# Optimization experiments

Hardware: AMD Instinct MI355X
Metric: run time of the kernel (lower is better)

Reference implementation:

```python
import jax, jax.numpy as jnp
import numpy as np

# --- constants mirroring ContextualAttention_Enhance defaults ---
C_IN = 64      # in_channels
C_I  = 16      # inter_channels
PS   = 7       # patch size (ps)
K    = 100     # top-k neighbors (k_s)
WS   = 21      # search window (ws)
S0   = 4       # query stride (stride0); stride1 = 1
SCALE = 10.0   # softmax_scale
B, H, W = 2, 96, 96
NH, NW = H // S0, W // S0
Q, HW, NC = NH * NW, H * W, WS * WS
P2, W2 = PS // 2, WS // 2


def _conv1x1(x, w, b):
    # x: [B,C,H,W], w: [Co,Ci], b: [Co]
    return jnp.einsum('bchw,oc->bohw', x, w) + b[None, :, None, None]


def _all_patches(x):
    # x: [C,H,W] -> centered ps x ps patches (clamped bounds) for every pixel: [HW, C*PS*PS]
    off = jnp.arange(PS) - P2
    ii = jnp.clip(jnp.arange(H)[:, None] + off, 0, H - 1)   # [H,PS]
    jj = jnp.clip(jnp.arange(W)[:, None] + off, 0, W - 1)   # [W,PS]
    p = x[:, ii[:, None, :, None], jj[None, :, None, :]]     # [C,H,W,PS,PS]
    return p.transpose(1, 2, 0, 3, 4).reshape(HW, -1)


def _query_pos():
    qi = jnp.repeat(jnp.arange(NH) * S0, NW)
    qj = jnp.tile(jnp.arange(NW) * S0, NH)
    return qi, qj


def _cand_idx():
    # flat pixel index of the WS x WS candidate centers around each query (clamped)
    qi, qj = _query_pos()
    d = jnp.arange(WS) - W2
    ci = jnp.clip(qi[:, None, None] + d[None, :, None], 0, H - 1)
    cj = jnp.clip(qj[:, None, None] + d[None, None, :], 0, W - 1)
    return (ci * W + cj).reshape(Q, NC)


def _attend(theta, phi, g):
    # theta/phi/g: [C_I,H,W]. Windowed top-k patch search + weighted patch-sum + fold.
    qi, qj = _query_pos()
    Qp = _all_patches(theta)[qi * W + qj]          # [Q, D] query patches
    Kp = _all_patches(phi)                          # [HW, D] key patches
    cand = _cand_idx()                              # [Q, NC]
    dfull = Qp @ Kp.T                               # [Q, HW] patch inner products
    dc = jnp.take_along_axis(dfull, cand, axis=1)   # [Q, NC] windowed scores
    topv, topi = jax.lax.top_k(dc, K)               # [Q, K]
    top = jnp.take_along_axis(cand, topi, axis=1)   # [Q, K] flat pixel inds
    wgt = jax.nn.softmax(SCALE * topv, axis=-1)     # [Q, K]
    Vp = _all_patches(g)                            # [HW, D] value patches
    z = jnp.einsum('qk,qkd->qd', wgt, Vp[top])      # weighted patch sum [Q, D]
    # fold: scatter-add patches back at query centers, normalize by overlap counts
    off = jnp.arange(PS) - P2
    pi = jnp.clip(qi[:, None, None] + off[:, None], 0, H - 1)
    pj = jnp.clip(qj[:, None, None] + off[None, :], 0, W - 1)
    pidx = (pi * W + pj).reshape(Q, PS * PS)
    zp = z.reshape(Q, C_I, PS * PS).transpose(1, 0, 2)        # [C_I,Q,PP]
    img = jnp.zeros((C_I, HW), z.dtype).at[:, pidx].add(zp)
    cnt = jnp.zeros((HW,), z.dtype).at[pidx.reshape(-1)].add(1.0)
    return (img / jnp.maximum(cnt, 1.0)[None]).reshape(C_I, H, W)


def setup_inputs() -> dict:
    key = jax.random.key(0)
    ks = jax.random.split(key, 12)
    s = 0.05
    return {
        'vid':     jax.random.normal(ks[0], (B, C_IN, H, W), jnp.float32),
        'w_theta': jax.random.normal(ks[1], (C_I, C_IN), jnp.float32) * s,
        'b_theta': jax.random.normal(ks[2], (C_I,), jnp.float32) * s,
        'w_phi':   jax.random.normal(ks[3], (C_I, C_IN), jnp.float32) * s,
        'b_phi':   jax.random.normal(ks[4], (C_I,), jnp.float32) * s,
        'w_g':     jax.random.normal(ks[5], (C_I, C_IN), jnp.float32) * s,
        'b_g':     jax.random.normal(ks[6], (C_I,), jnp.float32) * s,
        'w_w':     jax.random.normal(ks[7], (C_IN, C_I), jnp.float32) * s,
        'b_w':     jax.random.normal(ks[8], (C_IN,), jnp.float32) * s,
        'w_c33':   jax.random.normal(ks[9], (C_IN, 2 * C_IN), jnp.float32) * s,
        'b_c33':   jax.random.normal(ks[10], (C_IN,), jnp.float32) * s,
    }


def reference(vid, w_theta, b_theta, w_phi, b_phi, w_g, b_g, w_w, b_w, w_c33, b_c33):
    theta = _conv1x1(vid, w_theta, b_theta)   # [B,C_I,H,W]
    phi   = _conv1x1(vid, w_phi, b_phi)
    gval  = _conv1x1(vid, w_g, b_g)
    z = jax.vmap(_attend)(theta, phi, gval)   # [B,C_I,H,W]
    y = _conv1x1(z, w_w, b_w)                 # back to C_IN channels
    return _conv1x1(jnp.concatenate([y, vid], axis=1), w_c33, b_c33)
```

## Files before the change

kernel.cpp:

```cpp
#include <hip/hip_runtime.h>
#include <stdint.h>

typedef unsigned int u32;
typedef unsigned short u16;
typedef unsigned char u8;
typedef unsigned long long u64;
typedef _Float16 h2 __attribute__((ext_vector_type(2)));
typedef _Float16 h4 __attribute__((ext_vector_type(4)));
typedef _Float16 h8 __attribute__((ext_vector_type(8)));
typedef float f4 __attribute__((ext_vector_type(4)));

#define DEV __device__ __forceinline__

constexpr int HWp = 9216;

constexpr size_t O_I16 = 0;
constexpr size_t N_I16 = 2ull * 9216 * 48;
constexpr size_t O_Z   = O_I16 + N_I16 * 2;
constexpr size_t N_Z   = 2ull * 576 * 784;
constexpr size_t WS_NEED = O_Z + N_Z * 4;

DEV float bf2f(u16 x) { return __uint_as_float(((u32)x) << 16); }
DEV int clampi(int v, int lo, int hi) { return v < lo ? lo : (v > hi ? hi : v); }
DEV float cvt(const void* p, int i, bool f32) {
  return f32 ? ((const float*)p)[i] : bf2f(((const u16*)p)[i]);
}
DEV float dot2(h2 a, h2 b, float c) {
#if __has_builtin(__builtin_amdgcn_fdot2)
  return __builtin_amdgcn_fdot2(a, b, c, false);
#else
  return c + (float)a[0]*(float)b[0] + (float)a[1]*(float)b[1];
#endif
}
DEV float dot8(h8 a, h8 b, float c) {
  c = dot2(__builtin_shufflevector(a,a,0,1), __builtin_shufflevector(b,b,0,1), c);
  c = dot2(__builtin_shufflevector(a,a,2,3), __builtin_shufflevector(b,b,2,3), c);
  c = dot2(__builtin_shufflevector(a,a,4,5), __builtin_shufflevector(b,b,4,5), c);
  c = dot2(__builtin_shufflevector(a,a,6,7), __builtin_shufflevector(b,b,6,7), c);
  return c;
}
DEV bool hit256(const void* p, int tid) {
  u16 v = ((const u16*)p)[tid];
  return (((u32)v >> 7) & 0xFFu) >= 0xC8u;
}

__global__ __launch_bounds__(256, 2) void k1_conv(const void* vid, const void* wth, const void* bth,
    const void* wph, const void* bph, const void* wg, const void* bg, u8* ws)
{
  __shared__ float vidL[64 * 65];
  __shared__ float wL[48 * 65];
  __shared__ float bL[48];
  __shared__ __align__(16) _Float16 outL[64 * 48];
  __shared__ int redL[8];
  int tid = threadIdx.x;
  int g0 = blockIdx.x * 64;
  int b = g0 / HWp, px0 = g0 % HWp;

  {
    u64 b1 = __ballot(hit256(vid, tid));
    u64 b2 = __ballot(hit256(wth, tid));
    if ((tid & 63) == 0) { redL[tid >> 6] = __popcll(b1); redL[4 + (tid >> 6)] = __popcll(b2); }
  }
  __syncthreads();
  const bool vf = (redL[0] + redL[1] + redL[2] + redL[3]) >= 4;
  const bool wf = (redL[4] + redL[5] + redL[6] + redL[7]) >= 4;

  if (wf) {
    for (int e = tid; e < 768; e += 256) {
      int a = e >> 8, j = e & 255;
      int o = j >> 4, c4 = (j & 15) << 2;
      const float* src = (a == 0) ? (const float*)wth : (a == 1) ? (const float*)wph : (const float*)wg;
      f4 x = *(const f4*)(src + o*64 + c4);
#pragma unroll
      for (int jj = 0; jj < 4; ++jj) wL[(a*16 + o)*65 + c4 + jj] = x[jj];
    }
  } else {
    for (int e = tid; e < 384; e += 256) {
      int a = e >> 7, j = e & 127;
      int o = j >> 5, c2 = (j & 31) << 1;
      const u16* src = (a == 0) ? (const u16*)wth : (a == 1) ? (const u16*)wph : (const u16*)wg;
      u32 x = *(const u32*)(src + o*64 + c2);
      wL[(a*16 + o)*65 + c2]     = bf2f((u16)(x & 0xFFFF));
      wL[(a*16 + o)*65 + c2 + 1] = bf2f((u16)(x >> 16));
    }
  }
  if (tid < 48) bL[tid] = (tid < 16) ? cvt(bth, tid, wf) : (tid < 32) ? cvt(bph, tid-16, wf) : cvt(bg, tid-32, wf);
  if (vf) {
    const float* v = (const float*)vid;
    for (int e = tid; e < 1024; e += 256) {
      int c = e >> 4, qd = e & 15;
      f4 x = *(const f4*)(v + (size_t)(b*64 + c)*HWp + px0 + qd*4);
#pragma unroll
      for (int j = 0; j < 4; ++j) vidL[(qd*4 + j)*65 + c] = x[j];
    }
  } else {
    const u16* v = (const u16*)vid;
    for (int e = tid; e < 2048; e += 256) {
      int c = e >> 5, pp = (e & 31) * 2;
      u32 x = *(const u32*)(v + (size_t)(b*64 + c)*HWp + px0 + pp);
      vidL[pp*65 + c]     = bf2f((u16)(x & 0xFFFF));
      vidL[(pp+1)*65 + c] = bf2f((u16)(x >> 16));
    }
  }
  __syncthreads();

  int px = tid >> 2, h = tid & 3;
  float acc[12];
#pragma unroll
  for (int j = 0; j < 12; ++j) acc[j] = bL[h*12 + j];
  for (int c = 0; c < 64; ++c) {
    float v = vidL[px*65 + c];
#pragma unroll
    for (int j = 0; j < 12; ++j) acc[j] += wL[(h*12 + j)*65 + c] * v;
  }
#pragma unroll
  for (int j = 0; j < 12; ++j) outL[px*48 + h*12 + j] = (_Float16)acc[j];
  __syncthreads();

  _Float16* img = (_Float16*)(ws + O_I16);
  for (int e = tid; e < 384; e += 256) {
    int p = e / 6, seg = e % 6;
    *(h8*)(img + (size_t)(b*HWp + px0 + p)*48 + seg*8) = *(const h8*)&outL[p*48 + seg*8];
  }
}

__global__ __launch_bounds__(256, 2) void k2_attn(u8* ws)
{
  __shared__ __align__(16) _Float16 tA[729*8], tB[729*8];
  __shared__ __align__(16) _Float16 thA[49*8], thB[49*8];
  __shared__ float scL[441];
  __shared__ u8 crL[441], ccL[441];
  __shared__ u16 selL[100];
  __shared__ float wgtF[104];
  __shared__ u32 wgtH[100];

  const int tid = threadIdx.x, blk = blockIdx.x;
  const int b = blk / 576, q = blk % 576;
  const int qi = (q / 24) * 4, qj = (q % 24) * 4;
  const _Float16* I = (const _Float16*)(ws + O_I16) + (size_t)b * HWp * 48;

  for (int e = tid; e < 441; e += 256) {
    int d1 = e / 21, d2 = e % 21;
    crL[e] = (u8)clampi(qi + d1 - 10, 0, 95);
    ccL[e] = (u8)clampi(qj + d2 - 10, 0, 95);
  }
  for (int e = tid; e < 98; e += 256) {
    int p = e >> 1, hf = e & 1, di = p / 7, dj = p % 7;
    int ty = clampi(qi + di - 3, 0, 95), tx = clampi(qj + dj - 3, 0, 95);
    *(h8*)&(hf ? thB : thA)[p*8] = *(const h8*)(I + (size_t)(ty*96 + tx)*48 + hf*8);
  }
  for (int e = tid; e < 1458; e += 256) {
    int p = e >> 1, hf = e & 1, row = p / 27, col = p % 27;
    int gy = clampi(qi - 13 + row, 0, 95), gx = clampi(qj - 13 + col, 0, 95);
    *(h8*)&(hf ? tB : tA)[p*8] = *(const h8*)(I + (size_t)(gy*96 + gx)*48 + 16 + hf*8);
  }
  __syncthreads();

  {
    int u = tid;
    bool active = u < 231;
    int uu = active ? u : 0;
    int row = uu / 11, m = uu % 11;
    bool has1 = active && (m < 10);
    int d2_0 = (m < 10) ? 2*m : 20;
    int c0 = row*21 + d2_0;
    int cc0 = clampi(qj + d2_0 - 10, 0, 95);
    int s = clampi(qj + d2_0 - 9, 0, 95) - cc0;
    int cr0 = clampi(qi + row - 10, 0, 95);
    int ro[7], tw[8];
#pragma unroll
    for (int i = 0; i < 7; ++i) ro[i] = (clampi(cr0 + i - 3, 0, 95) - qi + 13) * 216;
#pragma unroll
    for (int j = 0; j < 8; ++j) {
      int t = clampi(cc0 + j - 3, 0, 95) - (qj - 13);
      tw[j] = (t > 26 ? 26 : t) * 8;
    }
    float a0A = 0.f, a0B = 0.f, a1A = 0.f, a1B = 0.f;
    for (int di = 0; di < 7; ++di) {
      int r = ro[di];
#pragma unroll
      for (int j = 0; j < 8; ++j) {
        h8 hA = *(const h8*)&tA[r + tw[j]];
        h8 hB = *(const h8*)&tB[r + tw[j]];
        if (j < 7) {
          int p0 = (di*7 + j)*8;
          a0A = dot8(*(const h8*)&thA[p0], hA, a0A);
          a0B = dot8(*(const h8*)&thB[p0], hB, a0B);
        }
        {
          int dj1 = j - s;
          bool v1 = has1 && (dj1 >= 0) && (dj1 <= 6);
          int p1 = (di*7 + clampi(dj1, 0, 6))*8;
          float rA = dot8(*(const h8*)&thA[p1], hA, a1A);
          float rB = dot8(*(const h8*)&thB[p1], hB, a1B);
          a1A = v1 ? rA : a1A;
          a1B = v1 ? rB : a1B;
        }
      }
    }
    if (active) scL[c0] = a0A + a0B;
    if (has1) scL[c0 + 1] = a1A + a1B;
  }
  __syncthreads();

  if (tid >= 64) {
    for (int e = tid - 64; e < 1458; e += 192) {
      int p = e >> 1, hf = e & 1, row = p / 27, col = p % 27;
      int gy = clampi(qi - 13 + row, 0, 95), gx = clampi(qj - 13 + col, 0, 95);
      *(h8*)&(hf ? tB : tA)[p*8] = *(const h8*)(I + (size_t)(gy*96 + gx)*48 + 32 + hf*8);
    }
  } else {
    const int lane = tid;
    const u64 lt = (1ull << lane) - 1ull;
    u64 kv[7];
#pragma unroll
    for (int s = 0; s < 7; ++s) {
      int idx = s * 64 + lane;
      if (idx < 441) {
        u32 bb = __float_as_uint(scL[idx]);
        u32 ob = (bb & 0x80000000u) ? ~bb : (bb | 0x80000000u);
        kv[s] = ((u64)ob << 9) | (u64)(511 - idx);
      } else kv[s] = 0ull;
    }
    u64 mx = kv[0];
#pragma unroll
    for (int s = 1; s < 7; ++s) mx = (kv[s] > mx) ? kv[s] : mx;
    for (int off = 1; off < 64; off <<= 1) { u64 o = __shfl_xor(mx, off, 64); mx = (o > mx) ? o : mx; }
    float vmax;
    { u32 ob = (u32)(mx >> 9); u32 bb = (ob & 0x80000000u) ? (ob & 0x7FFFFFFFu) : ~ob; vmax = __uint_as_float(bb); }
    u64 T = 0;
    for (int bit = 40; bit >= 0; --bit) {
      u64 cand = T | (1ull << bit);
      int cnt = 0;
#pragma unroll
      for (int s = 0; s < 7; ++s) cnt += __popcll(__ballot(kv[s] >= cand));
      if (cnt >= 100) T = cand;
    }
    float dloc = 0.f; int base = 0;
#pragma unroll
    for (int s = 0; s < 7; ++s) {
      bool incl = kv[s] >= T;
      u64 ib = __ballot(incl);
      if (incl) {
        int idx = 511 - (int)(kv[s] & 0x1FFull);
        u32 ob = (u32)(kv[s] >> 9);
        u32 bb = (ob & 0x80000000u) ? (ob & 0x7FFFFFFFu) : ~ob;
        float w = __expf(10.f * (__uint_as_float(bb) - vmax));
        int pos = base + __popcll(ib & lt);
        selL[pos] = (u16)idx;
        wgtF[pos] = w;
        dloc += w;
      }
      base += __popcll(ib);
    }
    for (int off = 1; off < 64; off <<= 1) dloc += __shfl_xor(dloc, off, 64);
    float inv = 1.f / dloc;
    for (int k = lane; k < 100; k += 64) {
      _Float16 wh = (_Float16)(wgtF[k] * inv);
      h2 p2; p2[0] = wh; p2[1] = wh;
      wgtH[k] = __builtin_bit_cast(u32, p2);
    }
  }
  __syncthreads();

  if (tid < 196) {
    int p = tid >> 2, cq = tid & 3;
    int di = p / 7, dj = p % 7;
    const _Float16* base = (cq < 2 ? tA : tB) + (cq & 1) * 4;
    h2 accA; accA[0] = (_Float16)0.f; accA[1] = (_Float16)0.f;
    h2 accB = accA;
    for (int k = 0; k < 100; ++k) {
      int si = selL[k];
      int ty = clampi((int)crL[si] + di - 3, 0, 95) - qi + 13;
      int tx = clampi((int)ccL[si] + dj - 3, 0, 95) - qj + 13;
      h4 g = *(const h4*)&base[(ty*27 + tx)*8];
      h2 w2 = __builtin_bit_cast(h2, wgtH[k]);
      accA += w2 * __builtin_shufflevector(g, g, 0, 1);
      accB += w2 * __builtin_shufflevector(g, g, 2, 3);
    }
    f4 zv; zv[0] = (float)accA[0]; zv[1] = (float)accA[1]; zv[2] = (float)accB[0]; zv[3] = (float)accB[1];
    *(f4*)((float*)(ws + O_Z) + (size_t)(b*576 + q)*784 + tid*4) = zv;
  }
}

__global__ __launch_bounds__(256, 2) void k3_out(const void* vid, const void* ww, const void* bw,
    const void* wc33, const void* bc33, float* out, const u8* ws)
{
  __shared__ float znL[16 * 96];
  __shared__ float vidL[64 * 96];
  __shared__ float WvL[32 * 65];
  __shared__ float WcL[32 * 65];
  __shared__ float wwL[1024];
  __shared__ float bwL[64];
  __shared__ float W1L[32 * 17];
  __shared__ float B0L[32];
  __shared__ u8 McL[96], MQL[384], MRL[384];
  __shared__ int redL[8];
  const int tid = threadIdx.x, blk = blockIdx.x;
  const int b = blk / 192, rem = blk % 192, y = rem >> 1, oh = (rem & 1) * 32;

  {
    u64 b1 = __ballot(hit256(vid, tid));
    u64 b2 = __ballot(hit256(wc33, tid));
    if ((tid & 63) == 0) { redL[tid >> 6] = __popcll(b1); redL[4 + (tid >> 6)] = __popcll(b2); }
  }
  __syncthreads();
  const bool vf = (redL[0] + redL[1] + redL[2] + redL[3]) >= 4;
  const bool wfl = (redL[4] + redL[5] + redL[6] + redL[7]) >= 4;

  if (wfl) {
    const float* wc = (const float*)wc33;
    for (int e = tid; e < 1024; e += 256) {
      int o = e >> 5, qd = e & 31;
      f4 x = *(const f4*)(wc + (oh + o)*128 + qd*4);
      int col = qd * 4;
      float* dst = (col < 64) ? &WcL[o*65 + col] : &WvL[o*65 + col - 64];
#pragma unroll
      for (int jj = 0; jj < 4; ++jj) dst[jj] = x[jj];
    }
    for (int e = tid; e < 256; e += 256) {
      f4 x = *(const f4*)((const float*)ww + e*4);
#pragma unroll
      for (int jj = 0; jj < 4; ++jj) wwL[e*4 + jj] = x[jj];
    }
  } else {
    const u16* wc = (const u16*)wc33;
    for (int e = tid; e < 2048; e += 256) {
      int o = e >> 6, q2 = e & 63;
      u32 x = *(const u32*)(wc + (oh + o)*128 + q2*2);
      int col = q2 * 2;
      float v0 = bf2f((u16)(x & 0xFFFF)), v1 = bf2f((u16)(x >> 16));
      if (col < 64) { WcL[o*65 + col] = v0; WcL[o*65 + col + 1] = v1; }
      else { WvL[o*65 + col - 64] = v0; WvL[o*65 + col - 63] = v1; }
    }
    for (int e = tid; e < 512; e += 256) {
      u32 x = *(const u32*)((const u16*)ww + e*2);
      wwL[e*2]     = bf2f((u16)(x & 0xFFFF));
      wwL[e*2 + 1] = bf2f((u16)(x >> 16));
    }
  }
  if (tid < 64) bwL[tid] = cvt(bw, tid, wfl);
  if (vf) {
    const float* v = (const float*)vid;
    for (int e = tid; e < 1536; e += 256) {
      int c = e / 24, qd = e % 24;
      *(f4*)&vidL[c*96 + qd*4] = *(const f4*)(v + (size_t)(b*64 + c)*HWp + y*96 + qd*4);
    }
  } else {
    const u16* v = (const u16*)vid;
    for (int e = tid; e < 3072; e += 256) {
      int c = e / 48, pp = (e % 48) * 2;
      u32 x = *(const u32*)(v + (size_t)(b*64 + c)*HWp + y*96 + pp);
      vidL[c*96 + pp]     = bf2f((u16)(x & 0xFFFF));
      vidL[c*96 + pp + 1] = bf2f((u16)(x >> 16));
    }
  }
  if (tid < 96) {
    int cnt = 0;
#pragma unroll 1
    for (int qy = 0; qy < 24; ++qy)
      for (int off = 0; off < 7; ++off) {
        int p = clampi(qy*4 + off - 3, 0, 95);
        if (p == tid && cnt < 4) { MQL[tid*4 + cnt] = (u8)qy; MRL[tid*4 + cnt] = (u8)off; ++cnt; }
      }
    McL[tid] = (u8)cnt;
  }
  __syncthreads();

  for (int e = tid; e < 512; e += 256) {
    int o = e >> 4, ci = e & 15;
    float s = 0.f;
    for (int c = 0; c < 64; ++c) s += WcL[o*65 + c] * wwL[c*16 + ci];
    W1L[o*17 + ci] = s;
  }
  if (tid < 32) {
    float s = cvt(bc33, oh + tid, wfl);
    for (int c = 0; c < 64; ++c) s += WcL[tid*65 + c] * bwL[c];
    B0L[tid] = s;
  }
  {
    const float* zG = (const float*)(ws + O_Z) + (size_t)b * 576 * 784;
    const int mcy = McL[y];
    for (int e = tid; e < 384; e += 256) {
      int x = e >> 2, cq = e & 3;
      int mcx = McL[x];
      f4 s = 0.f;
      for (int a = 0; a < mcy; ++a) {
        int qy = MQL[y*4 + a], rr = MRL[y*4 + a];
        size_t rowbase = ((size_t)qy * 24) * 784 + (size_t)(rr * 7) * 16 + cq * 4;
        for (int b2 = 0; b2 < mcx; ++b2) {
          int qx = MQL[x*4 + b2], ss = MRL[x*4 + b2];
          s += *(const f4*)(zG + rowbase + (size_t)qx * 784 + ss * 16);
        }
      }
      float invc = 1.f / (float)(mcy * mcx);
#pragma unroll
      for (int j = 0; j < 4; ++j) znL[(cq*4 + j)*96 + x] = s[j] * invc;
    }
  }
  __syncthreads();

  const int o = tid >> 3, xq = tid & 7;
  f4 a0, a1, a2;
  { float bz = B0L[o]; a0 = bz; a1 = bz; a2 = bz; }
  for (int ci = 0; ci < 16; ++ci) {
    float w = W1L[o*17 + ci];
    const f4* zp = (const f4*)&znL[ci*96 + xq*12];
    a0 += zp[0] * w; a1 += zp[1] * w; a2 += zp[2] * w;
  }
  for (int c = 0; c < 64; ++c) {
    float w = WvL[o*65 + c];
    const f4* vp = (const f4*)&vidL[c*96 + xq*12];
    a0 += vp[0] * w; a1 += vp[1] * w; a2 += vp[2] * w;
  }
  float* op = out + (size_t)(b*64 + oh + o) * HWp + y*96 + xq*12;
  *(f4*)(op + 0) = a0; *(f4*)(op + 4) = a1; *(f4*)(op + 8) = a2;
}

extern "C" void kernel_launch(void* const* d_in, const int* in_sizes, int n_in,
                              void* d_out, int out_size, void* d_ws, size_t ws_size,
                              hipStream_t stream)
{
  (void)in_sizes; (void)n_in; (void)out_size;
  const void* vid  = d_in[0];
  const void* wth  = d_in[1];
  const void* bth  = d_in[2];
  const void* wph  = d_in[3];
  const void* bph  = d_in[4];
  const void* wg   = d_in[5];
  const void* bg   = d_in[6];
  const void* ww   = d_in[7];
  const void* bw   = d_in[8];
  const void* wc33 = d_in[9];
  const void* bc33 = d_in[10];
  u8* ws = (u8*)d_ws;
  if (ws_size < WS_NEED) return;

  hipLaunchKernelGGL(k1_conv, dim3(288), dim3(256), 0, stream, vid, wth, bth, wph, bph, wg, bg, ws);
  hipLaunchKernelGGL(k2_attn, dim3(1152), dim3(256), 0, stream, ws);
  hipLaunchKernelGGL(k3_out, dim3(384), dim3(256), 0, stream, vid, ww, bw, wc33, bc33, (float*)d_out, ws);
}
```

Before: 156.6 us.

## Process two horizontally adjacent queries per attention block sharing one tile

Each k2_attn block now handles two neighbouring queries (4 pixels apart) and loads a 27x31 key/value tile shared between them, halving the grid to 576 blocks. Score computation and aggregation loop over both queries, and top-k selection runs on two wavefronts in parallel, one per query. This cuts redundant global tile loads and per-block setup, at the cost of more shared memory per block, serialized score/aggregation loops, and fewer blocks to fill the GPU.

```diff
diff --git a/kernel.cpp b/kernel.cpp
--- a/kernel.cpp
+++ b/kernel.cpp
@@ -126,55 +126,63 @@
 
 __global__ __launch_bounds__(256, 2) void k2_attn(u8* ws)
 {
-  __shared__ __align__(16) _Float16 tA[729*8], tB[729*8];
-  __shared__ __align__(16) _Float16 thA[49*8], thB[49*8];
-  __shared__ float scL[441];
-  __shared__ u8 crL[441], ccL[441];
-  __shared__ u16 selL[100];
-  __shared__ float wgtF[104];
-  __shared__ u32 wgtH[100];
+  __shared__ __align__(16) _Float16 tA[837*8], tB[837*8];
+  __shared__ __align__(16) _Float16 thA[2*49*8], thB[2*49*8];
+  __shared__ float scL[882];
+  __shared__ u8 crL[441];
+  __shared__ u8 ccL[882];
+  __shared__ u16 selL[200];
+  __shared__ float wgtF[2*104];
+  __shared__ u32 wgtH[200];
 
   const int tid = threadIdx.x, blk = blockIdx.x;
-  const int b = blk / 576, q = blk % 576;
-  const int qi = (q / 24) * 4, qj = (q % 24) * 4;
+  const int b = blk / 288, rem = blk % 288;
+  const int qi = (rem / 12) * 4, pair = rem % 12;
+  const int qjb = pair * 8;
+  const int qbase = (rem / 12) * 24 + pair * 2;
   const _Float16* I = (const _Float16*)(ws + O_I16) + (size_t)b * HWp * 48;
 
-  for (int e = tid; e < 441; e += 256) {
-    int d1 = e / 21, d2 = e % 21;
-    crL[e] = (u8)clampi(qi + d1 - 10, 0, 95);
-    ccL[e] = (u8)clampi(qj + d2 - 10, 0, 95);
-  }
-  for (int e = tid; e < 98; e += 256) {
-    int p = e >> 1, hf = e & 1, di = p / 7, dj = p % 7;
-    int ty = clampi(qi + di - 3, 0, 95), tx = clampi(qj + dj - 3, 0, 95);
-    *(h8*)&(hf ? thB : thA)[p*8] = *(const h8*)(I + (size_t)(ty*96 + tx)*48 + hf*8);
-  }
-  for (int e = tid; e < 1458; e += 256) {
-    int p = e >> 1, hf = e & 1, row = p / 27, col = p % 27;
-    int gy = clampi(qi - 13 + row, 0, 95), gx = clampi(qj - 13 + col, 0, 95);
+  for (int e = tid; e < 441; e += 256)
+    crL[e] = (u8)clampi(qi + e / 21 - 10, 0, 95);
+  for (int e = tid; e < 882; e += 256) {
+    int qq = e / 441, d2 = (e % 441) % 21;
+    ccL[e] = (u8)clampi(qjb + 4*qq + d2 - 10, 0, 95);
+  }
+  for (int e = tid; e < 196; e += 256) {
+    int qq = e / 98, r2 = e % 98;
+    int p = r2 >> 1, hf = r2 & 1, di = p / 7, dj = p % 7;
+    int ty = clampi(qi + di - 3, 0, 95), tx = clampi(qjb + 4*qq + dj - 3, 0, 95);
+    *(h8*)&(hf ? thB : thA)[qq*392 + p*8] = *(const h8*)(I + (size_t)(ty*96 + tx)*48 + hf*8);
+  }
+  for (int e = tid; e < 1674; e += 256) {
+    int p = e >> 1, hf = e & 1, row = p / 31, col = p % 31;
+    int gy = clampi(qi - 13 + row, 0, 95), gx = clampi(qjb - 13 + col, 0, 95);
     *(h8*)&(hf ? tB : tA)[p*8] = *(const h8*)(I + (size_t)(gy*96 + gx)*48 + 16 + hf*8);
   }
   __syncthreads();
 
-  {
-    int u = tid;
-    bool active = u < 231;
-    int uu = active ? u : 0;
+#pragma unroll 1
+  for (int qq = 0; qq < 2; ++qq) {
+    const int qje = qjb + 4*qq;
+    bool active = tid < 231;
+    int uu = active ? tid : 0;
     int row = uu / 11, m = uu % 11;
     bool has1 = active && (m < 10);
     int d2_0 = (m < 10) ? 2*m : 20;
     int c0 = row*21 + d2_0;
-    int cc0 = clampi(qj + d2_0 - 10, 0, 95);
-    int s = clampi(qj + d2_0 - 9, 0, 95) - cc0;
+    int cc0 = clampi(qje + d2_0 - 10, 0, 95);
+    int s = clampi(qje + d2_0 - 9, 0, 95) - cc0;
     int cr0 = clampi(qi + row - 10, 0, 95);
     int ro[7], tw[8];
 #pragma unroll
-    for (int i = 0; i < 7; ++i) ro[i] = (clampi(cr0 + i - 3, 0, 95) - qi + 13) * 216;
+    for (int i = 0; i < 7; ++i) ro[i] = (clampi(cr0 + i - 3, 0, 95) - qi + 13) * 248;
 #pragma unroll
     for (int j = 0; j < 8; ++j) {
-      int t = clampi(cc0 + j - 3, 0, 95) - (qj - 13);
-      tw[j] = (t > 26 ? 26 : t) * 8;
-    }
+      int t = clampi(cc0 + j - 3, 0, 95) - (qjb - 13);
+      tw[j] = (t > 30 ? 30 : t) * 8;
+    }
+    const _Float16* ta = thA + qq*392;
+    const _Float16* tb = thB + qq*392;
     float a0A = 0.f, a0B = 0.f, a1A = 0.f, a1B = 0.f;
     for (int di = 0; di < 7; ++di) {
       int r = ro[di];
@@ -184,47 +192,48 @@
         h8 hB = *(const h8*)&tB[r + tw[j]];
         if (j < 7) {
           int p0 = (di*7 + j)*8;
-          a0A = dot8(*(const h8*)&thA[p0], hA, a0A);
-          a0B = dot8(*(const h8*)&thB[p0], hB, a0B);
+          a0A = dot8(*(const h8*)&ta[p0], hA, a0A);
+          a0B = dot8(*(const h8*)&tb[p0], hB, a0B);
         }
         {
           int dj1 = j - s;
           bool v1 = has1 && (dj1 >= 0) && (dj1 <= 6);
           int p1 = (di*7 + clampi(dj1, 0, 6))*8;
-          float rA = dot8(*(const h8*)&thA[p1], hA, a1A);
-          float rB = dot8(*(const h8*)&thB[p1], hB, a1B);
+          float rA = dot8(*(const h8*)&ta[p1], hA, a1A);
+          float rB = dot8(*(const h8*)&tb[p1], hB, a1B);
           a1A = v1 ? rA : a1A;
           a1B = v1 ? rB : a1B;
         }
       }
     }
-    if (active) scL[c0] = a0A + a0B;
-    if (has1) scL[c0 + 1] = a1A + a1B;
-  }
-  __syncthreads();
-
-  if (tid >= 64) {
-    for (int e = tid - 64; e < 1458; e += 192) {
-      int p = e >> 1, hf = e & 1, row = p / 27, col = p % 27;
-      int gy = clampi(qi - 13 + row, 0, 95), gx = clampi(qj - 13 + col, 0, 95);
+    if (active) scL[qq*441 + c0] = a0A + a0B;
+    if (has1) scL[qq*441 + c0 + 1] = a1A + a1B;
+  }
+  __syncthreads();
+
+  if (tid >= 128) {
+    for (int e = tid - 128; e < 1674; e += 128) {
+      int p = e >> 1, hf = e & 1, row = p / 31, col = p % 31;
+      int gy = clampi(qi - 13 + row, 0, 95), gx = clampi(qjb - 13 + col, 0, 95);
       *(h8*)&(hf ? tB : tA)[p*8] = *(const h8*)(I + (size_t)(gy*96 + gx)*48 + 32 + hf*8);
     }
   } else {
-    const int lane = tid;
+    const int w = tid >> 6, lane = tid & 63;
+    const float* sc = scL + w*441;
     const u64 lt = (1ull << lane) - 1ull;
     u64 kv[7];
 #pragma unroll
-    for (int s = 0; s < 7; ++s) {
-      int idx = s * 64 + lane;
+    for (int sb = 0; sb < 7; ++sb) {
+      int idx = sb * 64 + lane;
       if (idx < 441) {
-        u32 bb = __float_as_uint(scL[idx]);
+        u32 bb = __float_as_uint(sc[idx]);
         u32 ob = (bb & 0x80000000u) ? ~bb : (bb | 0x80000000u);
-        kv[s] = ((u64)ob << 9) | (u64)(511 - idx);
-      } else kv[s] = 0ull;
+        kv[sb] = ((u64)ob << 9) | (u64)(511 - idx);
+      } else kv[sb] = 0ull;
     }
     u64 mx = kv[0];
 #pragma unroll
-    for (int s = 1; s < 7; ++s) mx = (kv[s] > mx) ? kv[s] : mx;
+    for (int sb = 1; sb < 7; ++sb) mx = (kv[sb] > mx) ? kv[sb] : mx;
     for (int off = 1; off < 64; off <<= 1) { u64 o = __shfl_xor(mx, off, 64); mx = (o > mx) ? o : mx; }
     float vmax;
     { u32 ob = (u32)(mx >> 9); u32 bb = (ob & 0x80000000u) ? (ob & 0x7FFFFFFFu) : ~ob; vmax = __uint_as_float(bb); }
@@ -233,53 +242,57 @@
       u64 cand = T | (1ull << bit);
       int cnt = 0;
 #pragma unroll
-      for (int s = 0; s < 7; ++s) cnt += __popcll(__ballot(kv[s] >= cand));
+      for (int sb = 0; sb < 7; ++sb) cnt += __popcll(__ballot(kv[sb] >= cand));
       if (cnt >= 100) T = cand;
     }
     float dloc = 0.f; int base = 0;
 #pragma unroll
-    for (int s = 0; s < 7; ++s) {
-      bool incl = kv[s] >= T;
+    for (int sb = 0; sb < 7; ++sb) {
+      bool incl = kv[sb] >= T;
       u64 ib = __ballot(incl);
       if (incl) {
-        int idx = 511 - (int)(kv[s] & 0x1FFull);
-        u32 ob = (u32)(kv[s] >> 9);
+        int idx = 511 - (int)(kv[sb] & 0x1FFull);
+        u32 ob = (u32)(kv[sb] >> 9);
         u32 bb = (ob & 0x80000000u) ? (ob & 0x7FFFFFFFu) : ~ob;
-        float w = __expf(10.f * (__uint_as_float(bb) - vmax));
+        float wv = __expf(10.f * (__uint_as_float(bb) - vmax));
         int pos = base + __popcll(ib & lt);
-        selL[pos] = (u16)idx;
-        wgtF[pos] = w;
-        dloc += w;
+        selL[w*100 + pos] = (u16)idx;
+        wgtF[w*104 + pos] = wv;
+        dloc += wv;
       }
       base += __popcll(ib);
     }
     for (int off = 1; off < 64; off <<= 1) dloc += __shfl_xor(dloc, off, 64);
     float inv = 1.f / dloc;
     for (int k = lane; k < 100; k += 64) {
-      _Float16 wh = (_Float16)(wgtF[k] * inv);
+      _Float16 wh = (_Float16)(wgtF[w*104 + k] * inv);
       h2 p2; p2[0] = wh; p2[1] = wh;
-      wgtH[k] = __builtin_bit_cast(u32, p2);
-    }
-  }
-  __syncthreads();
-
-  if (tid < 196) {
-    int p = tid >> 2, cq = tid & 3;
-    int di = p / 7, dj = p % 7;
-    const _Float16* base = (cq < 2 ? tA : tB) + (cq & 1) * 4;
-    h2 accA; accA[0] = (_Float16)0.f; accA[1] = (_Float16)0.f;
-    h2 accB = accA;
-    for (int k = 0; k < 100; ++k) {
-      int si = selL[k];
-      int ty = clampi((int)crL[si] + di - 3, 0, 95) - qi + 13;
-      int tx = clampi((int)ccL[si] + dj - 3, 0, 95) - qj + 13;
-      h4 g = *(const h4*)&base[(ty*27 + tx)*8];
-      h2 w2 = __builtin_bit_cast(h2, wgtH[k]);
-      accA += w2 * __builtin_shufflevector(g, g, 0, 1);
-      accB += w2 * __builtin_shufflevector(g, g, 2, 3);
-    }
-    f4 zv; zv[0] = (float)accA[0]; zv[1] = (float)accA[1]; zv[2] = (float)accB[0]; zv[3] = (float)accB[1];
-    *(f4*)((float*)(ws + O_Z) + (size_t)(b*576 + q)*784 + tid*4) = zv;
+      wgtH[w*100 + k] = __builtin_bit_cast(u32, p2);
+    }
+  }
+  __syncthreads();
+
+#pragma unroll 1
+  for (int qq = 0; qq < 2; ++qq) {
+    if (tid < 196) {
+      int p = tid >> 2, cq = tid & 3;
+      int di = p / 7, dj = p % 7;
+      const _Float16* base = (cq < 2 ? tA : tB) + (cq & 1) * 4;
+      const u8* cc = ccL + qq*441;
+      h2 accA; accA[0] = (_Float16)0.f; accA[1] = (_Float16)0.f;
+      h2 accB = accA;
+      for (int k = 0; k < 100; ++k) {
+        int si = selL[qq*100 + k];
+        int ty = clampi((int)crL[si] + di - 3, 0, 95) - qi + 13;
+        int tx = clampi((int)cc[si] + dj - 3, 0, 95) - (qjb - 13);
+        h4 g = *(const h4*)&base[(ty*31 + tx)*8];
+        h2 w2 = __builtin_bit_cast(h2, wgtH[qq*100 + k]);
+        accA += w2 * __builtin_shufflevector(g, g, 0, 1);
+        accB += w2 * __builtin_shufflevector(g, g, 2, 3);
+      }
+      f4 zv; zv[0] = (float)accA[0]; zv[1] = (float)accA[1]; zv[2] = (float)accB[0]; zv[3] = (float)accB[1];
+      *(f4*)((float*)(ws + O_Z) + (size_t)(b*576 + qbase + qq)*784 + tid*4) = zv;
+    }
   }
 }
 
@@ -437,6 +450,6 @@
   if (ws_size < WS_NEED) return;
 
   hipLaunchKernelGGL(k1_conv, dim3(288), dim3(256), 0, stream, vid, wth, bth, wph, bph, wg, bg, ws);
-  hipLaunchKernelGGL(k2_attn, dim3(1152), dim3(256), 0, stream, ws);
+  hipLaunchKernelGGL(k2_attn, dim3(576), dim3(256), 0, stream, ws);
   hipLaunchKernelGGL(k3_out, dim3(384), dim3(256), 0, stream, vid, ww, bw, wc33, bc33, (float*)d_out, ws);
 }
```

Result: slower. 161.3 us (+3.0%).
